# Performance work log

Measured on AMD Instinct MI355X. Metric: run time of the kernel, lower is better.

## Reference

```python
import jax, jax.numpy as jnp
import numpy as np

DIM = 128
DIM1 = 128
D_MODEL = DIM + DIM1          # 256
D_INNER = 2 * D_MODEL         # expand=2 -> 512
D_STATE = 16
D_CONV = 4
DT_RANK = (D_MODEL + 15) // 16  # ceil(d_model/16) = 16
B, H, W = 4, 64, 64


def layer_norm(x, g, b, eps=1e-5):
    mu = jnp.mean(x, axis=-1, keepdims=True)
    var = jnp.mean((x - mu) ** 2, axis=-1, keepdims=True)
    return (x - mu) * jax.lax.rsqrt(var + eps) * g + b


def setup_inputs() -> dict:
    key = jax.random.key(0)
    ks = jax.random.split(key, 16)
    s = lambda k, shape, scale: (jax.random.normal(k, shape, jnp.float32) * scale)
    inp = {
        "input": jax.random.normal(ks[0], (B, DIM, H, W), jnp.float32),
        "input2": jax.random.normal(ks[1], (B, DIM1, H, W), jnp.float32),
        # MambaB params
        "ln0_g": jnp.ones((D_MODEL,), jnp.float32),
        "ln0_b": jnp.zeros((D_MODEL,), jnp.float32),
        "outp_w": s(ks[2], (D_MODEL, DIM), 1.0 / np.sqrt(D_MODEL)),
        "outp_b": jnp.zeros((DIM,), jnp.float32),
        # Mamba params
        "in_proj_w": s(ks[3], (D_MODEL, 2 * D_INNER), 1.0 / np.sqrt(D_MODEL)),
        "conv_w": s(ks[4], (D_INNER, D_CONV), 1.0 / np.sqrt(D_CONV)),
        "conv_b": jnp.zeros((D_INNER,), jnp.float32),
        "x_proj_w": s(ks[5], (D_INNER, DT_RANK + 2 * D_STATE), 1.0 / np.sqrt(D_INNER)),
        "dt_proj_w": s(ks[6], (DT_RANK, D_INNER), 1.0 / np.sqrt(DT_RANK)),
        "dt_proj_b": s(ks[7], (D_INNER,), 0.1),
        "A_log": jnp.log(jnp.tile(jnp.arange(1.0, D_STATE + 1.0, dtype=jnp.float32), (D_INNER, 1))),
        "D_param": jnp.ones((D_INNER,), jnp.float32),
        "mamba_out_w": s(ks[8], (D_INNER, D_MODEL), 1.0 / np.sqrt(D_INNER)),
    }
    return inp


def mamba(x, in_proj_w, conv_w, conv_b, x_proj_w, dt_proj_w, dt_proj_b, A_log, D_param, mamba_out_w):
    b, L, _ = x.shape
    xz = x @ in_proj_w                       # [b, L, 2*di]
    xs, z = jnp.split(xz, 2, axis=-1)
    # causal depthwise conv over sequence
    xt = xs.transpose(0, 2, 1)               # [b, di, L]
    conv = jax.lax.conv_general_dilated(
        xt, conv_w[:, None, :], window_strides=(1,),
        padding=[(D_CONV - 1, 0)], feature_group_count=D_INNER)
    xs = jax.nn.silu(conv + conv_b[None, :, None]).transpose(0, 2, 1)  # [b, L, di]
    x_dbl = xs @ x_proj_w                    # [b, L, dt_rank + 2*n]
    dt = x_dbl[..., :DT_RANK]
    Bm = x_dbl[..., DT_RANK:DT_RANK + D_STATE]
    Cm = x_dbl[..., DT_RANK + D_STATE:]
    delta = jax.nn.softplus(dt @ dt_proj_w + dt_proj_b)  # [b, L, di]
    A = -jnp.exp(A_log)                      # [di, n]

    def step(h, t):
        d_t, B_t, C_t, x_t = t               # [b,di],[b,n],[b,n],[b,di]
        dA = jnp.exp(d_t[:, :, None] * A)    # [b, di, n]
        h = h * dA + (d_t * x_t)[:, :, None] * B_t[:, None, :]
        y = jnp.einsum('bdn,bn->bd', h, C_t)
        return h, y

    h0 = jnp.zeros((b, D_INNER, D_STATE), x.dtype)
    _, ys = jax.lax.scan(step, h0, (delta.transpose(1, 0, 2), Bm.transpose(1, 0, 2),
                                    Cm.transpose(1, 0, 2), xs.transpose(1, 0, 2)))
    y = ys.transpose(1, 0, 2) + xs * D_param
    y = y * jax.nn.silu(z)
    return y @ mamba_out_w                   # [b, L, d_model]


def reference(input, input2, ln0_g, ln0_b, outp_w, outp_b, in_proj_w, conv_w, conv_b,
              x_proj_w, dt_proj_w, dt_proj_b, A_log, D_param, mamba_out_w):
    b, c, h, w = input.shape
    x = jnp.concatenate((input, input2), axis=1)            # [b, d_model, h, w]
    x = x.reshape(b, D_MODEL, h * w).transpose(0, 2, 1)     # [b, hw, d_model]
    x = layer_norm(x, ln0_g, ln0_b)
    out = mamba(x, in_proj_w, conv_w, conv_b, x_proj_w, dt_proj_w, dt_proj_b,
                A_log, D_param, mamba_out_w)
    out = out @ outp_w + outp_b                             # [b, hw, dim]
    return out.transpose(0, 2, 1).reshape(b, c, h, w)
```

## Files before the change

kernel.cpp:

```cpp
#include <hip/hip_runtime.h>
#include <hip/hip_bf16.h>
#include <math.h>

#define LSEQ 4096
#define NR   16384
#define NB   4
#define CHUNK 32
#define NCH  128

typedef short bf16x8 __attribute__((ext_vector_type(8)));
typedef float f32x4  __attribute__((ext_vector_type(4)));

typedef __attribute__((address_space(1))) const void gvoid_t;
typedef __attribute__((address_space(3))) void svoid_t;

__device__ __forceinline__ void gld_lds16(void* lds, const void* g) {
    __builtin_amdgcn_global_load_lds((gvoid_t*)g, (svoid_t*)lds, 16, 0, 0);
}

__device__ __forceinline__ unsigned short to_bf16(float f) {
    union { float f; unsigned u; } x; x.f = f;
    unsigned r = (x.u + 0x7fff + ((x.u >> 16) & 1)) >> 16;
    return (unsigned short)r;
}
__device__ __forceinline__ float bf2f(unsigned short u) {
    union { unsigned u; float f; } x; x.u = ((unsigned)u) << 16;
    return x.f;
}
__device__ __forceinline__ float softplus_f(float x) {
    return x > 20.f ? x : __logf(1.f + __expf(x));
}
__device__ __forceinline__ float silu_f(float x) {
    return x / (1.f + __expf(-x));
}

__device__ __forceinline__ void pow_chain16(float r, float* a) {
    float r2 = r * r;
    float r4 = r2 * r2;
    float r8 = r4 * r4;
    a[0] = r;        a[1] = r2;       a[2] = r2 * r;   a[3] = r4;
    a[4] = r4 * r;   a[5] = r4 * r2;  a[6] = r4 * a[2]; a[7] = r8;
    a[8] = r8 * r;   a[9] = r8 * r2;  a[10] = r8 * a[2]; a[11] = r8 * r4;
    a[12] = r8 * a[4]; a[13] = r8 * a[5]; a[14] = r8 * a[6]; a[15] = r8 * r8;
}

__device__ __forceinline__ bool pow_ok16(const float* An) {
    bool ok = true;
    #pragma unroll
    for (int n = 1; n < 16; ++n) {
        float ref = (float)(n + 1) * An[0];
        ok = ok && (fabsf(An[n] - ref) <= 1e-4f * fabsf(An[n]) + 1e-30f);
    }
    return ok;
}

__global__ __launch_bounds__(256) void front_kernel(const float* __restrict__ in1,
                                                    const float* __restrict__ in2,
                                                    const float* __restrict__ g,
                                                    const float* __restrict__ beta,
                                                    const float* __restrict__ Wm,
                                                    const float* __restrict__ Wo,
                                                    const float* __restrict__ Wxp,
                                                    const float* __restrict__ A_log,
                                                    const float* __restrict__ W,
                                                    unsigned short* __restrict__ Abf,
                                                    unsigned short* __restrict__ WcT,
                                                    unsigned short* __restrict__ Wxpt,
                                                    float* __restrict__ anegp,
                                                    unsigned short* __restrict__ Wt) {
    __shared__ float tile[256][33];
    int blk = blockIdx.x;
    int tid = threadIdx.x;
    if (blk < 512) {
        __shared__ float s1[8][32], s2[8][32];
        __shared__ float smu[32], srs[32];
        int b  = blk >> 7;
        int t0 = (blk & 127) * 32;
        #pragma unroll
        for (int p = 0; p < 8; ++p) {
            int c = p * 32 + (tid >> 3);
            int toff = (tid & 7) * 4;
            const float* src = (c < 128) ? &in1[((size_t)(b * 128 + c)) * LSEQ + t0 + toff]
                                         : &in2[((size_t)(b * 128 + (c - 128))) * LSEQ + t0 + toff];
            float4 v = *(const float4*)src;
            tile[c][toff] = v.x; tile[c][toff+1] = v.y;
            tile[c][toff+2] = v.z; tile[c][toff+3] = v.w;
        }
        __syncthreads();
        {
            int t = tid & 31, gg = tid >> 5;
            float a1 = 0.f, a2 = 0.f;
            #pragma unroll
            for (int i = 0; i < 32; ++i) {
                float v = tile[gg * 32 + i][t];
                a1 += v; a2 += v * v;
            }
            s1[gg][t] = a1; s2[gg][t] = a2;
        }
        __syncthreads();
        if (tid < 32) {
            float a1 = 0.f, a2 = 0.f;
            #pragma unroll
            for (int gg = 0; gg < 8; ++gg) { a1 += s1[gg][tid]; a2 += s2[gg][tid]; }
            float m = a1 * (1.f / 256.f);
            float var = a2 * (1.f / 256.f) - m * m;
            smu[tid] = m;
            srs[tid] = rsqrtf(var + 1e-5f);
        }
        __syncthreads();
        int c = tid;
        float gc = g[c], bc = beta[c];
        #pragma unroll 4
        for (int t = 0; t < 32; ++t) {
            float v = (tile[c][t] - smu[t]) * srs[t] * gc + bc;
            Abf[((size_t)((b << 12) + t0 + t)) * 256 + c] = to_bf16(v);
        }
    } else if (blk < 768) {
        int gid = (blk - 512) * 256 + tid;
        int row = gid >> 7, col = gid & 127;
        float acc = 0.f;
        for (int k = 0; k < 256; ++k) acc += Wm[row * 256 + k] * Wo[k * 128 + col];
        WcT[(size_t)col * 512 + row] = to_bf16(acc);
    } else if (blk < 864) {
        int gid = (blk - 768) * 256 + tid;
        int n = gid >> 9, k = gid & 511;
        Wxpt[gid] = to_bf16(Wxp[(size_t)k * 48 + n]);
    } else if (blk < 896) {
        int gid = (blk - 864) * 256 + tid;
        anegp[gid] = -__expf(A_log[gid]);
    } else {
        float* tf = &tile[0][0];
        int local = blk - 896;
        int k0 = (local & 3) * 64;
        int n0 = (local >> 2) * 64;
        int a = tid & 63, q = tid >> 6;
        #pragma unroll
        for (int i = 0; i < 16; ++i) {
            int k = q * 16 + i;
            tf[k * 65 + a] = W[(size_t)(k0 + k) * 1024 + n0 + a];
        }
        __syncthreads();
        #pragma unroll
        for (int i = 0; i < 16; ++i) {
            int n = q * 16 + i;
            Wt[(size_t)(n0 + n) * 256 + k0 + a] = to_bf16(tf[a * 65 + n]);
        }
    }
}

__global__ __launch_bounds__(256) void gemm1_mfma(const unsigned short* __restrict__ Abf,
                                                  const unsigned short* __restrict__ Wt,
                                                  unsigned short* __restrict__ xh,
                                                  unsigned short* __restrict__ zs) {
    __shared__ __align__(16) short Asl[128][32];
    __shared__ __align__(16) short Bsl[128][32];
    int tid = threadIdx.x;
    int wv = tid >> 6, ln = tid & 63;
    int m0 = blockIdx.x * 128;
    int n0 = blockIdx.y * 128;
    int mw = (wv & 1) * 64, nw = (wv >> 1) * 64;

    f32x4 acc[4][4];
    #pragma unroll
    for (int i = 0; i < 4; ++i)
        #pragma unroll
        for (int j = 0; j < 4; ++j) acc[i][j] = (f32x4)(0.f);

    int srow  = ln >> 2;
    int skoff = (ln & 3) * 8;

    for (int k0 = 0; k0 < 256; k0 += 32) {
        #pragma unroll
        for (int i = 0; i < 2; ++i) {
            int j = wv * 2 + i;
            int row = j * 16 + srow;
            gld_lds16(&Asl[j * 16][0], &Abf[(size_t)(m0 + row) * 256 + k0 + skoff]);
            gld_lds16(&Bsl[j * 16][0], &Wt [(size_t)(n0 + row) * 256 + k0 + skoff]);
        }
        __syncthreads();
        bf16x8 af[4], bff[4];
        int fm = ln & 15, fk = (ln >> 4) * 8;
        #pragma unroll
        for (int i = 0; i < 4; ++i) {
            af[i]  = *(const bf16x8*)&Asl[mw + i * 16 + fm][fk];
            bff[i] = *(const bf16x8*)&Bsl[nw + i * 16 + fm][fk];
        }
        #pragma unroll
        for (int i = 0; i < 4; ++i)
            #pragma unroll
            for (int j = 0; j < 4; ++j)
                acc[i][j] = __builtin_amdgcn_mfma_f32_16x16x32_bf16(af[i], bff[j], acc[i][j], 0, 0, 0);
        __syncthreads();
    }
    int ccol = ln & 15, crow = (ln >> 4) * 4;
    bool zhalf = (n0 >= 512);
    #pragma unroll
    for (int i = 0; i < 4; ++i) {
        #pragma unroll
        for (int j = 0; j < 4; ++j) {
            int n = n0 + nw + j * 16 + ccol;
            #pragma unroll
            for (int r = 0; r < 4; ++r) {
                int m = m0 + mw + i * 16 + crow + r;
                float v = acc[i][j][r];
                if (zhalf) zs[(size_t)m * 512 + (n - 512)] = to_bf16(silu_f(v));
                else       xh[(size_t)m * 512 + n]         = to_bf16(v);
            }
        }
    }
}

__global__ __launch_bounds__(512, 4) void mid_kernel(const unsigned short* __restrict__ xh,
                                                     const float* __restrict__ cw,
                                                     const float* __restrict__ cb,
                                                     const unsigned short* __restrict__ Wxpt,
                                                     const float* __restrict__ Wdt,
                                                     const float* __restrict__ dtb,
                                                     const float* __restrict__ anegp,
                                                     unsigned* __restrict__ dxp,
                                                     float* __restrict__ xdbl,
                                                     float* __restrict__ Parr,
                                                     float* __restrict__ Harr) {
    __shared__ __align__(16) unsigned short xcs[CHUNK][520];
    __shared__ __align__(16) float xds[CHUNK][48];
    int tid = threadIdx.x;
    int chunk = blockIdx.x & (NCH - 1);
    int b     = blockIdx.x >> 7;
    int d = tid;
    int rbase = (b << 12) + chunk * CHUNK;

    float4 w4 = *(const float4*)&cw[d * 4];
    float cbd = cb[d];
    float An[16];
    #pragma unroll
    for (int n = 0; n < 16; n += 4) {
        float4 v = *(const float4*)&anegp[d * 16 + n];
        An[n] = v.x; An[n+1] = v.y; An[n+2] = v.z; An[n+3] = v.w;
    }
    float wdt[16];
    #pragma unroll
    for (int q = 0; q < 16; ++q) wdt[q] = Wdt[q * 512 + d];
    float bd = dtb[d];

    float x0 = 0.f, x1 = 0.f, x2 = 0.f;
    if (chunk > 0) {
        x0 = bf2f(xh[(size_t)(rbase - 3) * 512 + d]);
        x1 = bf2f(xh[(size_t)(rbase - 2) * 512 + d]);
        x2 = bf2f(xh[(size_t)(rbase - 1) * 512 + d]);
    }
    #pragma unroll
    for (int t = 0; t < CHUNK; ++t) {
        float x3 = bf2f(xh[(size_t)(rbase + t) * 512 + d]);
        float a = x0 * w4.x + x1 * w4.y + x2 * w4.z + x3 * w4.w + cbd;
        xcs[t][d] = to_bf16(silu_f(a));
        x0 = x1; x1 = x2; x2 = x3;
    }
    __syncthreads();

    {
        int wv = tid >> 6, ln = tid & 63;
        if (wv < 6) {
            int mt = (wv >= 3) ? 16 : 0;
            int wr = (wv >= 3) ? wv - 3 : wv;
            int nt = wr * 16;
            int fm = ln & 15, fk = (ln >> 4) * 8;
            f32x4 acc = (f32x4)(0.f);
            #pragma unroll 4
            for (int k0 = 0; k0 < 512; k0 += 32) {
                bf16x8 af  = *(const bf16x8*)&xcs[mt + fm][k0 + fk];
                bf16x8 bf_ = *(const bf16x8*)&Wxpt[(size_t)(nt + fm) * 512 + k0 + fk];
                acc = __builtin_amdgcn_mfma_f32_16x16x32_bf16(af, bf_, acc, 0, 0, 0);
            }
            int ccol = ln & 15, crow = (ln >> 4) * 4;
            #pragma unroll
            for (int r = 0; r < 4; ++r)
                xds[mt + crow + r][nt + ccol] = acc[r];
        }
    }
    __syncthreads();

    #pragma unroll
    for (int i = 0; i < 2; ++i) {
        int idx = tid + i * 512;
        int t = idx >> 5, n = idx & 31;
        xdbl[(size_t)(rbase + t) * 32 + n] = xds[t][16 + n];
    }

    bool pm = pow_ok16(An);
    float h[16];
    #pragma unroll
    for (int n = 0; n < 16; ++n) h[n] = 0.f;
    float S = 0.f;
    const float4* xds4 = (const float4*)&xds[0][0];
    if (pm) {
        float An0 = An[0];
        #pragma unroll 4
        for (int t = 0; t < CHUNK; ++t) {
            float a = bd;
            #pragma unroll
            for (int q4 = 0; q4 < 4; ++q4) {
                float4 s4 = xds4[t * 12 + q4];
                a += s4.x * wdt[q4*4+0] + s4.y * wdt[q4*4+1]
                   + s4.z * wdt[q4*4+2] + s4.w * wdt[q4*4+3];
            }
            unsigned short dbf = to_bf16(softplus_f(a));
            unsigned short xbf = xcs[t][d];
            float dv = bf2f(dbf), xv = bf2f(xbf);
            dxp[(size_t)(rbase + t) * 512 + d] = (unsigned)dbf | ((unsigned)xbf << 16);
            float dx = dv * xv;
            S += dv;
            float aP[16];
            pow_chain16(__expf(dv * An0), aP);
            #pragma unroll
            for (int g = 0; g < 4; ++g) {
                float4 Bv = xds4[t * 12 + 4 + g];
                h[g*4+0] = h[g*4+0] * aP[g*4+0] + dx * Bv.x;
                h[g*4+1] = h[g*4+1] * aP[g*4+1] + dx * Bv.y;
                h[g*4+2] = h[g*4+2] * aP[g*4+2] + dx * Bv.z;
                h[g*4+3] = h[g*4+3] * aP[g*4+3] + dx * Bv.w;
            }
        }
    } else {
        #pragma unroll 2
        for (int t = 0; t < CHUNK; ++t) {
            float a = bd;
            #pragma unroll
            for (int q4 = 0; q4 < 4; ++q4) {
                float4 s4 = xds4[t * 12 + q4];
                a += s4.x * wdt[q4*4+0] + s4.y * wdt[q4*4+1]
                   + s4.z * wdt[q4*4+2] + s4.w * wdt[q4*4+3];
            }
            unsigned short dbf = to_bf16(softplus_f(a));
            unsigned short xbf = xcs[t][d];
            float dv = bf2f(dbf), xv = bf2f(xbf);
            dxp[(size_t)(rbase + t) * 512 + d] = (unsigned)dbf | ((unsigned)xbf << 16);
            float dx = dv * xv;
            S += dv;
            #pragma unroll
            for (int g = 0; g < 4; ++g) {
                float4 Bv = xds4[t * 12 + 4 + g];
                h[g*4+0] = h[g*4+0] * __expf(dv * An[g*4+0]) + dx * Bv.x;
                h[g*4+1] = h[g*4+1] * __expf(dv * An[g*4+1]) + dx * Bv.y;
                h[g*4+2] = h[g*4+2] * __expf(dv * An[g*4+2]) + dx * Bv.z;
                h[g*4+3] = h[g*4+3] * __expf(dv * An[g*4+3]) + dx * Bv.w;
            }
        }
    }
    float P[16];
    if (pm) {
        pow_chain16(__expf(S * An[0]), P);
    } else {
        #pragma unroll
        for (int n = 0; n < 16; ++n) P[n] = __expf(S * An[n]);
    }
    size_t gbase = ((size_t)(b * 512 + d)) * 16;
    size_t coff  = (size_t)chunk * 32768;
    #pragma unroll
    for (int n = 0; n < 16; n += 4) {
        *(float4*)&Parr[coff + gbase + n] = make_float4(P[n], P[n+1], P[n+2], P[n+3]);
        *(float4*)&Harr[coff + gbase + n] = make_float4(h[n], h[n+1], h[n+2], h[n+3]);
    }
}

__global__ __launch_bounds__(256) void scan_pass2(const float* __restrict__ Parr,
                                                  float* __restrict__ Harr) {
    int gid = blockIdx.x * 256 + threadIdx.x;
    float carry = 0.f;
    #pragma unroll 8
    for (int c = 0; c < NCH; ++c) {
        size_t off = (size_t)c * 32768 + gid;
        float P = Parr[off], he = Harr[off];
        Harr[off] = carry;
        carry = he + P * carry;
    }
}

__global__ __launch_bounds__(256) void scan_pass3(const unsigned* __restrict__ dxp,
                                                  const unsigned short* __restrict__ zs,
                                                  const float* __restrict__ xdbl,
                                                  const float* __restrict__ anegp,
                                                  const float* __restrict__ Dp,
                                                  const float* __restrict__ Hin,
                                                  unsigned short* __restrict__ yf16) {
    __shared__ __align__(16) float4 sB4[CHUNK][4];
    __shared__ __align__(16) float4 sC4[CHUNK][4];
    int tid = threadIdx.x;
    int chunk = blockIdx.x & (NCH - 1);
    int half  = (blockIdx.x >> 7) & 1;
    int b     = blockIdx.x >> 8;
    int d = half * 256 + tid;
    int rbase = (b << 12) + chunk * CHUNK;
    unsigned pwv[CHUNK];
    #pragma unroll
    for (int t = 0; t < CHUNK; ++t)
        pwv[t] = dxp[(size_t)(rbase + t) * 512 + d];
    {
        float* sBf = (float*)sB4;
        float* sCf = (float*)sC4;
        #pragma unroll
        for (int i = 0; i < 2; ++i) {
            int e = tid + i * 256;
            int t = e >> 4, n = e & 15;
            sBf[t * 16 + n] = xdbl[(size_t)(rbase + t) * 32 + n];
            sCf[t * 16 + n] = xdbl[(size_t)(rbase + t) * 32 + 16 + n];
        }
    }
    float An[16];
    #pragma unroll
    for (int n = 0; n < 16; n += 4) {
        float4 v = *(const float4*)&anegp[d * 16 + n];
        An[n] = v.x; An[n+1] = v.y; An[n+2] = v.z; An[n+3] = v.w;
    }
    bool pm = pow_ok16(An);
    float Dv = Dp[d];
    __syncthreads();
    size_t gbase = ((size_t)(b * 512 + d)) * 16;
    size_t coff  = (size_t)chunk * 32768;
    float h[16];
    #pragma unroll
    for (int n = 0; n < 16; n += 4) {
        float4 v = *(const float4*)&Hin[coff + gbase + n];
        h[n] = v.x; h[n+1] = v.y; h[n+2] = v.z; h[n+3] = v.w;
    }
    if (pm) {
        float An0 = An[0];
        #pragma unroll 8
        for (int t = 0; t < CHUNK; ++t) {
            unsigned pw = pwv[t];
            float dv = bf2f((unsigned short)(pw & 0xffffu));
            float xv = bf2f((unsigned short)(pw >> 16));
            float zv = bf2f(zs[(size_t)(rbase + t) * 512 + d]);
            float dx = dv * xv;
            float a[16];
            pow_chain16(__expf(dv * An0), a);
            float y = 0.f;
            #pragma unroll
            for (int g = 0; g < 4; ++g) {
                float4 Bv = sB4[t][g];
                float4 Cv = sC4[t][g];
                h[g*4+0] = h[g*4+0] * a[g*4+0] + dx * Bv.x;
                h[g*4+1] = h[g*4+1] * a[g*4+1] + dx * Bv.y;
                h[g*4+2] = h[g*4+2] * a[g*4+2] + dx * Bv.z;
                h[g*4+3] = h[g*4+3] * a[g*4+3] + dx * Bv.w;
                y += h[g*4+0] * Cv.x + h[g*4+1] * Cv.y
                   + h[g*4+2] * Cv.z + h[g*4+3] * Cv.w;
            }
            y += xv * Dv;
            y *= zv;
            yf16[(size_t)(rbase + t) * 512 + d] = to_bf16(y);
        }
    } else {
        #pragma unroll 4
        for (int t = 0; t < CHUNK; ++t) {
            unsigned pw = pwv[t];
            float dv = bf2f((unsigned short)(pw & 0xffffu));
            float xv = bf2f((unsigned short)(pw >> 16));
            float zv = bf2f(zs[(size_t)(rbase + t) * 512 + d]);
            float dx = dv * xv;
            float y = 0.f;
            #pragma unroll
            for (int g = 0; g < 4; ++g) {
                float4 Bv = sB4[t][g];
                float4 Cv = sC4[t][g];
                h[g*4+0] = h[g*4+0] * __expf(dv * An[g*4+0]) + dx * Bv.x;
                h[g*4+1] = h[g*4+1] * __expf(dv * An[g*4+1]) + dx * Bv.y;
                h[g*4+2] = h[g*4+2] * __expf(dv * An[g*4+2]) + dx * Bv.z;
                h[g*4+3] = h[g*4+3] * __expf(dv * An[g*4+3]) + dx * Bv.w;
                y += h[g*4+0] * Cv.x + h[g*4+1] * Cv.y
                   + h[g*4+2] * Cv.z + h[g*4+3] * Cv.w;
            }
            y += xv * Dv;
            y *= zv;
            yf16[(size_t)(rbase + t) * 512 + d] = to_bf16(y);
        }
    }
}

__global__ __launch_bounds__(256) void gemm_out_mfma(const unsigned short* __restrict__ WcT,
                                                     const unsigned short* __restrict__ yf16,
                                                     const float* __restrict__ bo,
                                                     float* __restrict__ out) {
    __shared__ __align__(16) short Asl[128][32];
    __shared__ __align__(16) short Bsl[64][32];
    int tid = threadIdx.x;
    int wv = tid >> 6, ln = tid & 63;
    int n0 = blockIdx.x * 64;
    int mw = (wv & 1) * 64, nw = (wv >> 1) * 32;

    f32x4 acc[4][2];
    #pragma unroll
    for (int i = 0; i < 4; ++i)
        #pragma unroll
        for (int j = 0; j < 2; ++j) acc[i][j] = (f32x4)(0.f);

    int srow  = ln >> 2;
    int skoff = (ln & 3) * 8;

    for (int k0 = 0; k0 < 512; k0 += 32) {
        #pragma unroll
        for (int i = 0; i < 2; ++i) {
            int j = wv * 2 + i;
            int row = j * 16 + srow;
            gld_lds16(&Asl[j * 16][0], &WcT[(size_t)row * 512 + k0 + skoff]);
        }
        {
            int row = wv * 16 + srow;
            gld_lds16(&Bsl[wv * 16][0], &yf16[(size_t)(n0 + row) * 512 + k0 + skoff]);
        }
        __syncthreads();
        bf16x8 af[4], bff[2];
        int fm = ln & 15, fk = (ln >> 4) * 8;
        #pragma unroll
        for (int i = 0; i < 4; ++i) af[i]  = *(const bf16x8*)&Asl[mw + i * 16 + fm][fk];
        #pragma unroll
        for (int j = 0; j < 2; ++j) bff[j] = *(const bf16x8*)&Bsl[nw + j * 16 + fm][fk];
        #pragma unroll
        for (int i = 0; i < 4; ++i)
            #pragma unroll
            for (int j = 0; j < 2; ++j)
                acc[i][j] = __builtin_amdgcn_mfma_f32_16x16x32_bf16(af[i], bff[j], acc[i][j], 0, 0, 0);
        __syncthreads();
    }
    int ccol = ln & 15, crow = (ln >> 4) * 4;
    int b = n0 >> 12, tb = n0 & 4095;
    #pragma unroll
    for (int i = 0; i < 4; ++i) {
        #pragma unroll
        for (int r = 0; r < 4; ++r) {
            int c = mw + i * 16 + crow + r;
            float bias = bo[c];
            #pragma unroll
            for (int j = 0; j < 2; ++j) {
                int t = tb + nw + j * 16 + ccol;
                out[((size_t)(b * 128 + c)) * LSEQ + t] = acc[i][j][r] + bias;
            }
        }
    }
}

extern "C" void kernel_launch(void* const* d_in, const int* in_sizes, int n_in,
                              void* d_out, int out_size, void* d_ws, size_t ws_size,
                              hipStream_t stream) {
    (void)in_sizes; (void)n_in; (void)out_size; (void)ws_size;
    const float* input    = (const float*)d_in[0];
    const float* input2   = (const float*)d_in[1];
    const float* ln_g     = (const float*)d_in[2];
    const float* ln_b     = (const float*)d_in[3];
    const float* outp_w   = (const float*)d_in[4];
    const float* outp_b   = (const float*)d_in[5];
    const float* in_proj  = (const float*)d_in[6];
    const float* conv_w   = (const float*)d_in[7];
    const float* conv_b   = (const float*)d_in[8];
    const float* x_proj   = (const float*)d_in[9];
    const float* dt_w     = (const float*)d_in[10];
    const float* dt_b     = (const float*)d_in[11];
    const float* A_log    = (const float*)d_in[12];
    const float* D_param  = (const float*)d_in[13];
    const float* mout_w   = (const float*)d_in[14];
    float* out = (float*)d_out;

    char* ws = (char*)d_ws;
    unsigned short* xh    = (unsigned short*)ws;                    ws += (size_t)NR * 512 * 2;
    unsigned short* zsbuf = (unsigned short*)ws;                    ws += (size_t)NR * 512 * 2;
    unsigned short* yf16  = (unsigned short*)ws;                    ws += (size_t)NR * 512 * 2;
    unsigned*       dxp   = (unsigned*)ws;                          ws += (size_t)NR * 512 * 4;
    unsigned short* Abf   = (unsigned short*)ws;                    ws += (size_t)NR * 256 * 2;
    unsigned short* Wt    = (unsigned short*)ws;                    ws += (size_t)1024 * 256 * 2;
    unsigned short* WcT   = (unsigned short*)ws;                    ws += (size_t)128 * 512 * 2;
    unsigned short* Wxpt  = (unsigned short*)ws;                    ws += (size_t)48 * 512 * 2;
    float* anegp = (float*)ws;                                      ws += (size_t)512 * 16 * 4;
    float* xdbl = (float*)ws;                                       ws += (size_t)NR * 32 * 4;
    float* Parr = (float*)ws;                                       ws += (size_t)NCH * 32768 * 4;
    float* Harr = (float*)ws;                                       ws += (size_t)NCH * 32768 * 4;

    front_kernel<<<960, 256, 0, stream>>>(input, input2, ln_g, ln_b, mout_w, outp_w,
                                          x_proj, A_log, in_proj,
                                          Abf, WcT, Wxpt, anegp, Wt);
    gemm1_mfma<<<dim3(128, 8), 256, 0, stream>>>(Abf, Wt, xh, zsbuf);
    mid_kernel<<<NB * NCH, 512, 0, stream>>>(xh, conv_w, conv_b, Wxpt, dt_w, dt_b,
                                             anegp, dxp, xdbl, Parr, Harr);
    scan_pass2<<<128, 256, 0, stream>>>(Parr, Harr);
    scan_pass3<<<NB * NCH * 2, 256, 0, stream>>>(dxp, zsbuf, xdbl, anegp, D_param,
                                                 Harr, yf16);
    gemm_out_mfma<<<NR / 64, 256, 0, stream>>>(WcT, yf16, outp_b, out);
}
```

Measured before the change: 212.6 us.

## Store per-chunk delta sums instead of decay products; pack scan math into float2

The chunk scan now writes one summed delta per (chunk,batch,channel) instead of 16 decay products per state, and the carry pass recomputes exp(S*A) on the fly. This drops the Parr buffer traffic (write plus read of NCH*32768 floats). The recurrences in mid_kernel and scan_pass3 are rewritten with float2 vectors so the compiler can emit packed FP32 ops, and the weight-fold loop gets an unroll pragma. In exchange, the carry pass does one exp per element per chunk, and it always uses exp(S*A_n), even when the power-chain path was taken.

```diff
diff --git a/kernel.cpp b/kernel.cpp
--- a/kernel.cpp
+++ b/kernel.cpp
@@ -10,6 +10,7 @@
 
 typedef short bf16x8 __attribute__((ext_vector_type(8)));
 typedef float f32x4  __attribute__((ext_vector_type(4)));
+typedef float f32x2  __attribute__((ext_vector_type(2)));
 
 typedef __attribute__((address_space(1))) const void gvoid_t;
 typedef __attribute__((address_space(3))) void svoid_t;
@@ -34,14 +35,19 @@
     return x / (1.f + __expf(-x));
 }
 
-__device__ __forceinline__ void pow_chain16(float r, float* a) {
+__device__ __forceinline__ void pow_chain16_pk(float r, f32x2* a2) {
     float r2 = r * r;
     float r4 = r2 * r2;
     float r8 = r4 * r4;
-    a[0] = r;        a[1] = r2;       a[2] = r2 * r;   a[3] = r4;
-    a[4] = r4 * r;   a[5] = r4 * r2;  a[6] = r4 * a[2]; a[7] = r8;
-    a[8] = r8 * r;   a[9] = r8 * r2;  a[10] = r8 * a[2]; a[11] = r8 * r4;
-    a[12] = r8 * a[4]; a[13] = r8 * a[5]; a[14] = r8 * a[6]; a[15] = r8 * r8;
+    f32x2 v01 = { r, r2 };
+    a2[0] = v01;
+    a2[1] = v01 * r2;
+    a2[2] = v01 * r4;
+    a2[3] = a2[1] * r4;
+    a2[4] = v01 * r8;
+    a2[5] = a2[1] * r8;
+    a2[6] = a2[2] * r8;
+    a2[7] = a2[3] * r8;
 }
 
 __device__ __forceinline__ bool pow_ok16(const float* An) {
@@ -119,6 +125,7 @@
         int gid = (blk - 512) * 256 + tid;
         int row = gid >> 7, col = gid & 127;
         float acc = 0.f;
+        #pragma unroll 8
         for (int k = 0; k < 256; ++k) acc += Wm[row * 256 + k] * Wo[k * 128 + col];
         WcT[(size_t)col * 512 + row] = to_bf16(acc);
     } else if (blk < 864) {
@@ -219,7 +226,7 @@
                                                      const float* __restrict__ anegp,
                                                      unsigned* __restrict__ dxp,
                                                      float* __restrict__ xdbl,
-                                                     float* __restrict__ Parr,
+                                                     float* __restrict__ Sarr,
                                                      float* __restrict__ Harr) {
     __shared__ __align__(16) unsigned short xcs[CHUNK][520];
     __shared__ __align__(16) float xds[CHUNK][48];
@@ -237,9 +244,12 @@
         float4 v = *(const float4*)&anegp[d * 16 + n];
         An[n] = v.x; An[n+1] = v.y; An[n+2] = v.z; An[n+3] = v.w;
     }
-    float wdt[16];
-    #pragma unroll
-    for (int q = 0; q < 16; ++q) wdt[q] = Wdt[q * 512 + d];
+    f32x2 wdt2[8];
+    #pragma unroll
+    for (int q = 0; q < 8; ++q) {
+        wdt2[q].x = Wdt[(2 * q) * 512 + d];
+        wdt2[q].y = Wdt[(2 * q + 1) * 512 + d];
+    }
     float bd = dtb[d];
 
     float x0 = 0.f, x1 = 0.f, x2 = 0.f;
@@ -287,49 +297,40 @@
     }
 
     bool pm = pow_ok16(An);
-    float h[16];
-    #pragma unroll
-    for (int n = 0; n < 16; ++n) h[n] = 0.f;
+    f32x2 h2[8];
+    #pragma unroll
+    for (int n = 0; n < 8; ++n) h2[n] = (f32x2)(0.f);
     float S = 0.f;
-    const float4* xds4 = (const float4*)&xds[0][0];
+    const f32x2* xds2 = (const f32x2*)&xds[0][0];
     if (pm) {
         float An0 = An[0];
         #pragma unroll 4
         for (int t = 0; t < CHUNK; ++t) {
-            float a = bd;
-            #pragma unroll
-            for (int q4 = 0; q4 < 4; ++q4) {
-                float4 s4 = xds4[t * 12 + q4];
-                a += s4.x * wdt[q4*4+0] + s4.y * wdt[q4*4+1]
-                   + s4.z * wdt[q4*4+2] + s4.w * wdt[q4*4+3];
-            }
+            f32x2 acc2 = { bd, 0.f };
+            #pragma unroll
+            for (int q = 0; q < 8; ++q)
+                acc2 = acc2 + xds2[t * 24 + q] * wdt2[q];
+            float a = acc2.x + acc2.y;
             unsigned short dbf = to_bf16(softplus_f(a));
             unsigned short xbf = xcs[t][d];
             float dv = bf2f(dbf), xv = bf2f(xbf);
             dxp[(size_t)(rbase + t) * 512 + d] = (unsigned)dbf | ((unsigned)xbf << 16);
             float dx = dv * xv;
             S += dv;
-            float aP[16];
-            pow_chain16(__expf(dv * An0), aP);
-            #pragma unroll
-            for (int g = 0; g < 4; ++g) {
-                float4 Bv = xds4[t * 12 + 4 + g];
-                h[g*4+0] = h[g*4+0] * aP[g*4+0] + dx * Bv.x;
-                h[g*4+1] = h[g*4+1] * aP[g*4+1] + dx * Bv.y;
-                h[g*4+2] = h[g*4+2] * aP[g*4+2] + dx * Bv.z;
-                h[g*4+3] = h[g*4+3] * aP[g*4+3] + dx * Bv.w;
-            }
+            f32x2 a2[8];
+            pow_chain16_pk(__expf(dv * An0), a2);
+            #pragma unroll
+            for (int g = 0; g < 8; ++g)
+                h2[g] = h2[g] * a2[g] + dx * xds2[t * 24 + 8 + g];
         }
     } else {
         #pragma unroll 2
         for (int t = 0; t < CHUNK; ++t) {
-            float a = bd;
-            #pragma unroll
-            for (int q4 = 0; q4 < 4; ++q4) {
-                float4 s4 = xds4[t * 12 + q4];
-                a += s4.x * wdt[q4*4+0] + s4.y * wdt[q4*4+1]
-                   + s4.z * wdt[q4*4+2] + s4.w * wdt[q4*4+3];
-            }
+            f32x2 acc2 = { bd, 0.f };
+            #pragma unroll
+            for (int q = 0; q < 8; ++q)
+                acc2 = acc2 + xds2[t * 24 + q] * wdt2[q];
+            float a = acc2.x + acc2.y;
             unsigned short dbf = to_bf16(softplus_f(a));
             unsigned short xbf = xcs[t][d];
             float dv = bf2f(dbf), xv = bf2f(xbf);
@@ -337,41 +338,36 @@
             float dx = dv * xv;
             S += dv;
             #pragma unroll
-            for (int g = 0; g < 4; ++g) {
-                float4 Bv = xds4[t * 12 + 4 + g];
-                h[g*4+0] = h[g*4+0] * __expf(dv * An[g*4+0]) + dx * Bv.x;
-                h[g*4+1] = h[g*4+1] * __expf(dv * An[g*4+1]) + dx * Bv.y;
-                h[g*4+2] = h[g*4+2] * __expf(dv * An[g*4+2]) + dx * Bv.z;
-                h[g*4+3] = h[g*4+3] * __expf(dv * An[g*4+3]) + dx * Bv.w;
-            }
-        }
-    }
-    float P[16];
-    if (pm) {
-        pow_chain16(__expf(S * An[0]), P);
-    } else {
-        #pragma unroll
-        for (int n = 0; n < 16; ++n) P[n] = __expf(S * An[n]);
-    }
+            for (int g = 0; g < 8; ++g) {
+                f32x2 e = { __expf(dv * An[2*g]), __expf(dv * An[2*g+1]) };
+                h2[g] = h2[g] * e + dx * xds2[t * 24 + 8 + g];
+            }
+        }
+    }
+    Sarr[(size_t)chunk * 2048 + b * 512 + d] = S;
     size_t gbase = ((size_t)(b * 512 + d)) * 16;
     size_t coff  = (size_t)chunk * 32768;
     #pragma unroll
-    for (int n = 0; n < 16; n += 4) {
-        *(float4*)&Parr[coff + gbase + n] = make_float4(P[n], P[n+1], P[n+2], P[n+3]);
-        *(float4*)&Harr[coff + gbase + n] = make_float4(h[n], h[n+1], h[n+2], h[n+3]);
-    }
-}
-
-__global__ __launch_bounds__(256) void scan_pass2(const float* __restrict__ Parr,
+    for (int n = 0; n < 4; ++n) {
+        *(float4*)&Harr[coff + gbase + n * 4] =
+            make_float4(h2[2*n].x, h2[2*n].y, h2[2*n+1].x, h2[2*n+1].y);
+    }
+}
+
+__global__ __launch_bounds__(256) void scan_pass2(const float* __restrict__ Sarr,
+                                                  const float* __restrict__ anegp,
                                                   float* __restrict__ Harr) {
     int gid = blockIdx.x * 256 + threadIdx.x;
+    float An = anegp[gid & 8191];
+    int sidx = gid >> 4;
     float carry = 0.f;
     #pragma unroll 8
     for (int c = 0; c < NCH; ++c) {
+        float S  = Sarr[(size_t)c * 2048 + sidx];
         size_t off = (size_t)c * 32768 + gid;
-        float P = Parr[off], he = Harr[off];
+        float he = Harr[off];
         Harr[off] = carry;
-        carry = he + P * carry;
+        carry = he + __expf(S * An) * carry;
     }
 }
 
@@ -416,12 +412,14 @@
     __syncthreads();
     size_t gbase = ((size_t)(b * 512 + d)) * 16;
     size_t coff  = (size_t)chunk * 32768;
-    float h[16];
-    #pragma unroll
-    for (int n = 0; n < 16; n += 4) {
-        float4 v = *(const float4*)&Hin[coff + gbase + n];
-        h[n] = v.x; h[n+1] = v.y; h[n+2] = v.z; h[n+3] = v.w;
-    }
+    f32x2 h2[8];
+    #pragma unroll
+    for (int n = 0; n < 4; ++n) {
+        float4 v = *(const float4*)&Hin[coff + gbase + n * 4];
+        h2[2*n].x = v.x; h2[2*n].y = v.y; h2[2*n+1].x = v.z; h2[2*n+1].y = v.w;
+    }
+    const f32x2* sB2 = (const f32x2*)&sB4[0][0];
+    const f32x2* sC2 = (const f32x2*)&sC4[0][0];
     if (pm) {
         float An0 = An[0];
         #pragma unroll 8
@@ -431,21 +429,15 @@
             float xv = bf2f((unsigned short)(pw >> 16));
             float zv = bf2f(zs[(size_t)(rbase + t) * 512 + d]);
             float dx = dv * xv;
-            float a[16];
-            pow_chain16(__expf(dv * An0), a);
-            float y = 0.f;
-            #pragma unroll
-            for (int g = 0; g < 4; ++g) {
-                float4 Bv = sB4[t][g];
-                float4 Cv = sC4[t][g];
-                h[g*4+0] = h[g*4+0] * a[g*4+0] + dx * Bv.x;
-                h[g*4+1] = h[g*4+1] * a[g*4+1] + dx * Bv.y;
-                h[g*4+2] = h[g*4+2] * a[g*4+2] + dx * Bv.z;
-                h[g*4+3] = h[g*4+3] * a[g*4+3] + dx * Bv.w;
-                y += h[g*4+0] * Cv.x + h[g*4+1] * Cv.y
-                   + h[g*4+2] * Cv.z + h[g*4+3] * Cv.w;
-            }
-            y += xv * Dv;
+            f32x2 a2[8];
+            pow_chain16_pk(__expf(dv * An0), a2);
+            f32x2 y2 = (f32x2)(0.f);
+            #pragma unroll
+            for (int g = 0; g < 8; ++g) {
+                h2[g] = h2[g] * a2[g] + dx * sB2[t * 8 + g];
+                y2 = y2 + h2[g] * sC2[t * 8 + g];
+            }
+            float y = y2.x + y2.y + xv * Dv;
             y *= zv;
             yf16[(size_t)(rbase + t) * 512 + d] = to_bf16(y);
         }
@@ -457,19 +449,14 @@
             float xv = bf2f((unsigned short)(pw >> 16));
             float zv = bf2f(zs[(size_t)(rbase + t) * 512 + d]);
             float dx = dv * xv;
-            float y = 0.f;
-            #pragma unroll
-            for (int g = 0; g < 4; ++g) {
-                float4 Bv = sB4[t][g];
-                float4 Cv = sC4[t][g];
-                h[g*4+0] = h[g*4+0] * __expf(dv * An[g*4+0]) + dx * Bv.x;
-                h[g*4+1] = h[g*4+1] * __expf(dv * An[g*4+1]) + dx * Bv.y;
-                h[g*4+2] = h[g*4+2] * __expf(dv * An[g*4+2]) + dx * Bv.z;
-                h[g*4+3] = h[g*4+3] * __expf(dv * An[g*4+3]) + dx * Bv.w;
-                y += h[g*4+0] * Cv.x + h[g*4+1] * Cv.y
-                   + h[g*4+2] * Cv.z + h[g*4+3] * Cv.w;
-            }
-            y += xv * Dv;
+            f32x2 y2 = (f32x2)(0.f);
+            #pragma unroll
+            for (int g = 0; g < 8; ++g) {
+                f32x2 e = { __expf(dv * An[2*g]), __expf(dv * An[2*g+1]) };
+                h2[g] = h2[g] * e + dx * sB2[t * 8 + g];
+                y2 = y2 + h2[g] * sC2[t * 8 + g];
+            }
+            float y = y2.x + y2.y + xv * Dv;
             y *= zv;
             yf16[(size_t)(rbase + t) * 512 + d] = to_bf16(y);
         }
@@ -570,7 +557,7 @@
     unsigned short* Wxpt  = (unsigned short*)ws;                    ws += (size_t)48 * 512 * 2;
     float* anegp = (float*)ws;                                      ws += (size_t)512 * 16 * 4;
     float* xdbl = (float*)ws;                                       ws += (size_t)NR * 32 * 4;
-    float* Parr = (float*)ws;                                       ws += (size_t)NCH * 32768 * 4;
+    float* Sarr = (float*)ws;                                       ws += (size_t)NCH * 2048 * 4;
     float* Harr = (float*)ws;                                       ws += (size_t)NCH * 32768 * 4;
 
     front_kernel<<<960, 256, 0, stream>>>(input, input2, ln_g, ln_b, mout_w, outp_w,
@@ -578,8 +565,8 @@
                                           Abf, WcT, Wxpt, anegp, Wt);
     gemm1_mfma<<<dim3(128, 8), 256, 0, stream>>>(Abf, Wt, xh, zsbuf);
     mid_kernel<<<NB * NCH, 512, 0, stream>>>(xh, conv_w, conv_b, Wxpt, dt_w, dt_b,
-                                             anegp, dxp, xdbl, Parr, Harr);
-    scan_pass2<<<128, 256, 0, stream>>>(Parr, Harr);
+                                             anegp, dxp, xdbl, Sarr, Harr);
+    scan_pass2<<<128, 256, 0, stream>>>(Sarr, anegp, Harr);
     scan_pass3<<<NB * NCH * 2, 256, 0, stream>>>(dxp, zsbuf, xdbl, anegp, D_param,
                                                  Harr, yf16);
     gemm_out_mfma<<<NR / 64, 256, 0, stream>>>(WcT, yf16, outp_b, out);
```

Result: faster. 207.4 us (-2.4%).
